# Kernel tuning notes

Measured on AMD Instinct MI355X. Metric: run time of the kernel, lower is better.

The kernel has to match this reference:

```python
import jax, jax.numpy as jnp
import numpy as np
from jax import lax

N = 4096   # total tree nodes in the forest
K = 8      # max children per side (left / right)
D = 512    # lstm_hid_dims (node embedding / enc output dim)
H = 512    # chain_hid_dims (chain LSTM hidden dim)


def _make_children(seed):
    # child indices strictly less than the parent index -> ascending node
    # order is a valid post-order (children encoded before parents).
    r = np.random.default_rng(seed)
    ch = np.full((N, K), -1, np.int64)
    for i in range(1, N):
        n = int(r.integers(0, K + 1))
        if n > 0:
            ch[i, :n] = r.integers(0, i, size=n)
    return jnp.asarray(ch)


def setup_inputs() -> dict:
    key = jax.random.key(0)
    ks = jax.random.split(key, 12)
    s = 1.0 / np.sqrt(H)
    f32 = jnp.float32
    return {
        "x0": jax.random.normal(ks[0], (N, D), f32),
        "Wl_ih": jax.random.normal(ks[1], (4 * H, D), f32) * s,
        "Wl_hh": jax.random.normal(ks[2], (4 * H, H), f32) * s,
        "bl_ih": jax.random.normal(ks[3], (4 * H,), f32) * s,
        "bl_hh": jax.random.normal(ks[4], (4 * H,), f32) * s,
        "Wr_ih": jax.random.normal(ks[5], (4 * H, D), f32) * s,
        "Wr_hh": jax.random.normal(ks[6], (4 * H, H), f32) * s,
        "br_ih": jax.random.normal(ks[7], (4 * H,), f32) * s,
        "br_hh": jax.random.normal(ks[8], (4 * H,), f32) * s,
        "W_enc": jax.random.normal(ks[9], (D, 2 * H), f32) * s,
        "b_enc": jax.random.normal(ks[10], (D,), f32) * s,
        "left_children": _make_children(1),
        "right_children": _make_children(2),
    }


def _lstm_chain(x_seq, mask, Wih, Whh, bih, bhh):
    """Masked torch-style LSTM over x_seq [L, D]; returns last valid hidden [H]."""
    def step(carry, xm):
        h, c = carry
        x, m = xm
        g = x @ Wih.T + bih + h @ Whh.T + bhh  # [4H], gate order i,f,g,o
        i, f, gg, o = jnp.split(g, 4)
        c_new = jax.nn.sigmoid(f) * c + jax.nn.sigmoid(i) * jnp.tanh(gg)
        h_new = jax.nn.sigmoid(o) * jnp.tanh(c_new)
        h = jnp.where(m, h_new, h)
        c = jnp.where(m, c_new, c)
        return (h, c), None

    z = jnp.zeros((H,), x_seq.dtype)
    (h, _), _ = lax.scan(step, (z, z), (x_seq, mask))
    return h


def reference(x0, Wl_ih, Wl_hh, bl_ih, bl_hh, Wr_ih, Wr_hh, br_ih, br_hh,
              W_enc, b_enc, left_children, right_children):
    # Bottom-up pass: process nodes in post-order (ascending index). For each
    # node: left-chain LSTM over [own embedding, left child encodings...],
    # right-chain likewise, then enc = tanh(Linear(concat(hl, hr))).
    def node_step(ctx, inputs):
        i, xi, lch, rch = inputs
        lmask = lch >= 0
        rmask = rch >= 0
        lvecs = jnp.where(lmask[:, None], ctx[jnp.clip(lch, 0)], 0.0)  # [K, D]
        rvecs = jnp.where(rmask[:, None], ctx[jnp.clip(rch, 0)], 0.0)
        true1 = jnp.ones((1,), bool)
        hl = _lstm_chain(jnp.concatenate([xi[None], lvecs], 0),
                         jnp.concatenate([true1, lmask]),
                         Wl_ih, Wl_hh, bl_ih, bl_hh)
        hr = _lstm_chain(jnp.concatenate([xi[None], rvecs], 0),
                         jnp.concatenate([true1, rmask]),
                         Wr_ih, Wr_hh, br_ih, br_hh)
        enc = jnp.tanh(jnp.concatenate([hl, hr]) @ W_enc.T + b_enc)  # [D]
        return ctx.at[i].set(enc), None

    ctx0 = jnp.zeros((N, D), x0.dtype)
    idx = jnp.arange(N)
    ctx, _ = lax.scan(node_step, ctx0, (idx, x0, left_children, right_children))
    return ctx  # [N, D] per-node encodings (context_vec after bottom_up)
```

## Files before the change

kernel.cpp:

```cpp
#include <hip/hip_runtime.h>
#include <math.h>

#define NN 4096
#define KK 8
#define DD 512
#define HH 512
#define NB 256
#define TPB 1024
#define NXCD 8
#define MAXT 4096
#define ENTCAP 40960
#define ENCCAP 16384
#define NNHH ((size_t)NN * HH)

typedef float v2f __attribute__((ext_vector_type(2)));

#define OFF_CTRL 0
#define OFF_HDR  8192
#define OFF_TCNT (OFF_HDR + 256)
#define OFF_TOFF (OFF_TCNT + 4 * MAXT)
#define OFF_TCUR (OFF_TOFF + 4 * MAXT)
#define OFF_ECNT (OFF_TCUR + 4 * MAXT)
#define OFF_EOFF (OFF_ECNT + 4 * MAXT)
#define OFF_ECUR (OFF_EOFF + 4 * MAXT)
#define OFF_LIST (OFF_ECUR + 4 * MAXT)
#define OFF_XL   (OFF_LIST + 4 * ENTCAP)
#define OFF_XR   (OFF_XL + 4 * ENTCAP)
#define OFF_ENC  (OFF_XR + 4 * ENTCAP)
#define OFF_H    (OFF_ENC + 4 * ENCCAP)
#define OFF_C    (OFF_H + 4 * 2 * 2 * NN * HH)
#define WS_ZERO_BYTES 8192

__device__ __forceinline__ float fast_tanh2x(float two_x) {
    return 1.0f - 2.0f * __builtin_amdgcn_rcpf(__expf(two_x) + 1.0f);
}

__device__ __forceinline__ void glds16(const float* g, float* l) {
    typedef __attribute__((address_space(1))) const void GV;
    typedef __attribute__((address_space(3))) void LV;
    __builtin_amdgcn_global_load_lds((GV*)g, (LV*)l, 16, 0, 0);
}

__device__ __forceinline__ void coh_store(float* p, float v) {
    __hip_atomic_store(p, v, __ATOMIC_RELAXED, __HIP_MEMORY_SCOPE_AGENT);
}
__device__ __forceinline__ v2f ldb2(const float* p) {
    unsigned long long raw = __hip_atomic_load((const unsigned long long*)p,
                                               __ATOMIC_RELAXED, __HIP_MEMORY_SCOPE_AGENT);
    union { unsigned long long u; v2f f; } c; c.u = raw; return c.f;
}

__global__ void __launch_bounds__(1024)
sched_kernel(const int* __restrict__ lch, const int* __restrict__ rch, char* ws) {
    const int t = threadIdx.x;
    int* hdr   = (int*)(ws + OFF_HDR);
    int* gcnt  = (int*)(ws + OFF_TCNT);
    int* goff  = (int*)(ws + OFF_TOFF);
    int* gcur  = (int*)(ws + OFF_TCUR);
    int* gecnt = (int*)(ws + OFF_ECNT);
    int* geoff = (int*)(ws + OFF_EOFF);
    int* gecur = (int*)(ws + OFF_ECUR);
    int* list  = (int*)(ws + OFF_LIST);
    int* xl    = (int*)(ws + OFF_XL);
    int* xr    = (int*)(ws + OFF_XR);
    int* enc   = (int*)(ws + OFF_ENC);

    __shared__ int s_meta[NN];
    __shared__ int s_start[NN];
    __shared__ int s_seg[1024];
    __shared__ int s_un, s_nt;

    for (int j = t; j < MAXT; j += 1024) { gcnt[j] = 0; gcur[j] = 0; gecnt[j] = 0; gecur[j] = 0; }
    if (t == 0) s_nt = 0;
    for (int i = t; i < NN; i += 1024) {
        int ll = 1, lr = 1; bool has = false;
#pragma unroll
        for (int k = 0; k < KK; ++k) {
            if (lch[i * KK + k] >= 0) { ll = k + 2; has = true; }
            if (rch[i * KK + k] >= 0) { lr = k + 2; has = true; }
        }
        const int L = ll > lr ? ll : lr;
        s_meta[i]  = ll | (lr << 4) | (L << 8);
        s_start[i] = has ? -1 : 0;
    }
    __syncthreads();

    for (;;) {
        if (t == 0) s_un = 0;
        __syncthreads();
        int myUn = 0;
        for (int i = t; i < NN; i += 1024) {
            if (s_start[i] < 0) {
                int mx = 0; bool ok = true;
#pragma unroll
                for (int k = 0; k < KK; ++k) {
                    int c = lch[i * KK + k];
                    if (c >= 0) {
                        const int st = s_start[c];
                        if (st < 0) ok = false;
                        else { const int v = st + ((s_meta[c] >> 8) & 0xF) - k; if (v > mx) mx = v; }
                    }
                    c = rch[i * KK + k];
                    if (c >= 0) {
                        const int st = s_start[c];
                        if (st < 0) ok = false;
                        else { const int v = st + ((s_meta[c] >> 8) & 0xF) - k; if (v > mx) mx = v; }
                    }
                }
                if (ok) s_start[i] = mx; else ++myUn;
            }
        }
        if (myUn) atomicAdd(&s_un, myUn);
        __syncthreads();
        if (s_un == 0) break;
        __syncthreads();
    }

    for (int i = t; i < NN; i += 1024)
        atomicMax(&s_nt, s_start[i] + ((s_meta[i] >> 8) & 0xF) + 1);
    __syncthreads();
    const int nt = s_nt;
    if (t == 0) hdr[0] = nt;
    for (int i = t; i < NN; i += 1024) {
        const int s = s_start[i], L = (s_meta[i] >> 8) & 0xF;
        for (int q = 0; q < L; ++q) atomicAdd(&gcnt[s + q], 1);
        atomicAdd(&gecnt[s + L], 1);
    }
    __syncthreads();

    auto scan4 = [&](int* cnt, int* off) {
        const int per = (nt + 1023) >> 10;
        const int lo = t * per, hi = (lo + per < nt) ? lo + per : nt;
        int sum = 0;
        for (int j = lo; j < hi; ++j) sum += (cnt[j] + 3) & ~3;
        s_seg[t] = sum;
        __syncthreads();
        if (t == 0) { int run = 0; for (int k = 0; k < 1024; ++k) { const int v = s_seg[k]; s_seg[k] = run; run += v; } }
        __syncthreads();
        int run = s_seg[t];
        for (int j = lo; j < hi; ++j) { off[j] = run; run += (cnt[j] + 3) & ~3; }
        __syncthreads();
    };
    scan4(gcnt, goff);
    scan4(gecnt, geoff);

    for (int i = t; i < NN; i += 1024) {
        const int m = s_meta[i], s = s_start[i];
        const int ll = m & 0xF, lr = (m >> 4) & 0xF, L = (m >> 8) & 0xF;
        for (int q = 0; q < L; ++q) {
            const int pos = goff[s + q] + atomicAdd(&gcur[s + q], 1);
            list[pos] = i | (q << 12) | (ll << 16) | (lr << 20);
            xl[pos] = (q == 0) ? i : ((q < ll) ? lch[i * KK + q - 1] : -1);
            xr[pos] = (q == 0) ? i : ((q < lr) ? rch[i * KK + q - 1] : -1);
        }
        const int ep = geoff[s + L] + atomicAdd(&gecur[s + L], 1);
        enc[ep] = i | (ll << 12) | (lr << 16);
    }
}

__device__ __forceinline__ void grid_barrier(int* ctrl, int blk, int xcd, int target) {
    __syncthreads();
    if (blk == 0) {
        const int t = threadIdx.x;
        if (t < 64) {
            if (t == 0)
                __hip_atomic_store(ctrl + 0, target, __ATOMIC_RELAXED, __HIP_MEMORY_SCOPE_AGENT);
            int spin = 0;
            for (;;) {
                const int m0 = __hip_atomic_load(ctrl + t * 4 + 0, __ATOMIC_RELAXED, __HIP_MEMORY_SCOPE_AGENT);
                const int m1 = __hip_atomic_load(ctrl + t * 4 + 1, __ATOMIC_RELAXED, __HIP_MEMORY_SCOPE_AGENT);
                const int m2 = __hip_atomic_load(ctrl + t * 4 + 2, __ATOMIC_RELAXED, __HIP_MEMORY_SCOPE_AGENT);
                const int m3 = __hip_atomic_load(ctrl + t * 4 + 3, __ATOMIC_RELAXED, __HIP_MEMORY_SCOPE_AGENT);
                const bool ok = (m0 >= target) & (m1 >= target) & (m2 >= target) & (m3 >= target);
                if (__all(ok)) break;
                if (++spin > 64) __builtin_amdgcn_s_sleep(16);
                else             __builtin_amdgcn_s_sleep(1);
            }
            if (t < NXCD)
                __hip_atomic_store(ctrl + 512 + t * 16, target, __ATOMIC_RELAXED, __HIP_MEMORY_SCOPE_AGENT);
        }
    } else {
        if (threadIdx.x == 0) {
            __hip_atomic_store(ctrl + blk, target, __ATOMIC_RELAXED, __HIP_MEMORY_SCOPE_AGENT);
            int spin = 0;
            while (__hip_atomic_load(ctrl + 512 + xcd * 16, __ATOMIC_RELAXED, __HIP_MEMORY_SCOPE_AGENT) < target) {
                if (++spin > 64) __builtin_amdgcn_s_sleep(16);
                else             __builtin_amdgcn_s_sleep(1);
            }
        }
    }
    __syncthreads();
}

__global__ void __launch_bounds__(TPB, 1)
tree_lstm_kernel(const float* __restrict__ x0,
                 const float* __restrict__ Wl_ih, const float* __restrict__ Wl_hh,
                 const float* __restrict__ bl_ih, const float* __restrict__ bl_hh,
                 const float* __restrict__ Wr_ih, const float* __restrict__ Wr_hh,
                 const float* __restrict__ br_ih, const float* __restrict__ br_hh,
                 const float* __restrict__ W_enc, const float* __restrict__ b_enc,
                 float* ctx, char* ws) {
    const int tid  = threadIdx.x;
    const int wv   = tid >> 6;
    const int wave = (blockIdx.x * TPB + tid) >> 6;
    const int lane = tid & 63;
    const int u    = wave & 511;
    const int side = (wave >> 9) & 1;
    const int p    = (wave >> 10) & 3;
    const int egrp = (wave >> 9) & 7;
    const int xcd  = blockIdx.x & (NXCD - 1);
    const int u0b  = (blockIdx.x * 16) & 511;

    int*   ctrl  = (int*)(ws + OFF_CTRL);
    int*   hdr   = (int*)(ws + OFF_HDR);
    int*   gcnt  = (int*)(ws + OFF_TCNT);
    int*   goff  = (int*)(ws + OFF_TOFF);
    int*   gecnt = (int*)(ws + OFF_ECNT);
    int*   geoff = (int*)(ws + OFF_EOFF);
    int*   list  = (int*)(ws + OFF_LIST);
    int*   xlidx = (int*)(ws + OFF_XL);
    int*   xridx = (int*)(ws + OFF_XR);
    int*   encl  = (int*)(ws + OFF_ENC);
    float* hbuf  = (float*)(ws + OFF_H);
    float* cbuf  = (float*)(ws + OFF_C);

    __shared__ float s_x[2][8][512];
    __shared__ float s_h[2][8][512];
    __shared__ float s_c[2][8][16];
    __shared__ float s_pad[5120];

    const float* Wih = side ? Wr_ih : Wl_ih;
    const float* Whh = side ? Wr_hh : Wl_hh;
    const float* bih = side ? br_ih : bl_ih;
    const float* bhh = side ? br_hh : bl_hh;

    v2f wih2[4][4], whh2[4][4];
#pragma unroll
    for (int g = 0; g < 4; ++g) {
        const size_t row = (size_t)g * HH + u;
        const float4 wa = *(const float4*)(Wih + row * DD + lane * 4);
        const float4 wb = *(const float4*)(Wih + row * DD + 256 + lane * 4);
        wih2[g][0] = (v2f){wa.x, wa.y}; wih2[g][1] = (v2f){wa.z, wa.w};
        wih2[g][2] = (v2f){wb.x, wb.y}; wih2[g][3] = (v2f){wb.z, wb.w};
        const float4 ha = *(const float4*)(Whh + row * HH + lane * 4);
        const float4 hb = *(const float4*)(Whh + row * HH + 256 + lane * 4);
        whh2[g][0] = (v2f){ha.x, ha.y}; whh2[g][1] = (v2f){ha.z, ha.w};
        whh2[g][2] = (v2f){hb.x, hb.y}; whh2[g][3] = (v2f){hb.z, hb.w};
    }
    const float bsumL = bih[(size_t)(lane & 3) * HH + u] + bhh[(size_t)(lane & 3) * HH + u];
    v2f wenc2[8];
#pragma unroll
    for (int j = 0; j < 4; ++j) {
        const float4 t = *(const float4*)(W_enc + (size_t)u * (2 * HH) + lane * 16 + j * 4);
        wenc2[j * 2 + 0] = (v2f){t.x, t.y};
        wenc2[j * 2 + 1] = (v2f){t.z, t.w};
    }
    const float bencv = b_enc[u];

    float* cb = cbuf + (size_t)side * NNHH;
    const int* xq = side ? xridx : xlidx;
    const int nt = hdr[0];
    if (nt < 0) ((volatile float*)s_pad)[tid] = 0.f;
    int bnum = 0;

    for (int tk = 0; tk < nt; ++tk) {
        const int cnt  = gcnt[tk],  off  = goff[tk];
        const int ecnt = gecnt[tk], eoff = geoff[tk];
        const int limit = off + cnt;

        const int slotBase = off + p * 8;
        const int nch = (limit > slotBase) ? ((limit - slotBase + 31) >> 5) : 0;

        v2f ph0, ph1, ph2, ph3, pc;
        bool pact = false;

        auto issue = [&](int buf, int chS) {
            pact = false;
            if (wv < 8) {
                const int e = chS + wv;
                if (e < limit) {
                    const int ent  = list[e];
                    const int q    = (ent >> 12) & 0xF;
                    const int xsrc = xq[e];
                    if (xsrc >= 0) {
                        const float* xrow = ((q == 0) ? x0 : ctx) + (size_t)xsrc * DD + lane * 4;
                        glds16(xrow,       &s_x[buf][wv][0]);
                        glds16(xrow + 256, &s_x[buf][wv][256]);
                        if (q > 0) {
                            pact = true;
                            const int i = ent & 0xFFF;
                            const float* hr = hbuf + (size_t)(((q & 1) ^ 1) * 2 + side) * NNHH
                                            + (size_t)i * HH + lane * 4;
                            ph0 = ldb2(hr);       ph1 = ldb2(hr + 2);
                            ph2 = ldb2(hr + 256); ph3 = ldb2(hr + 258);
                            if (lane < 8)
                                pc = ldb2(cb + (size_t)i * HH + u0b + lane * 2);
                        }
                    }
                }
            }
        };
        auto writeb = [&](int buf) {
            if (pact) {
                *(v2f*)&s_h[buf][wv][lane * 4]       = ph0;
                *(v2f*)&s_h[buf][wv][lane * 4 + 2]   = ph1;
                *(v2f*)&s_h[buf][wv][lane * 4 + 256] = ph2;
                *(v2f*)&s_h[buf][wv][lane * 4 + 258] = ph3;
                if (lane < 8)
                    *(v2f*)&s_c[buf][wv][lane * 2] = pc;
            }
        };

        if (nch > 0) { issue(0, slotBase); writeb(0); }
        for (int c = 0; c < nch; ++c) {
            __syncthreads();
            const int chS = slotBase + (c << 5);
            if (c + 1 < nch) issue((c + 1) & 1, chS + 32);
            const int bb = c & 1;

            const int4 eA = *(const int4*)(list + chS);
            const int4 eB = *(const int4*)(list + chS + 4);
            const int4 cA = *(const int4*)(xq + chS);
            const int4 cB = *(const int4*)(xq + chS + 4);
            const int ei[8] = {eA.x, eA.y, eA.z, eA.w, eB.x, eB.y, eB.z, eB.w};
            const int ci[8] = {cA.x, cA.y, cA.z, cA.w, cB.x, cB.y, cB.z, cB.w};
            bool act[8];
#pragma unroll
            for (int j = 0; j < 8; ++j)
                act[j] = (chS + j < limit) && (ci[j] >= 0);

#pragma unroll
            for (int j = 0; j < 8; ++j) {
                if (!act[j]) continue;
                const int ent = ei[j];
                const int i   = ent & 0xFFF;
                const int qj  = (ent >> 12) & 0xF;
                const float cpj = (qj > 0) ? s_c[bb][j][wv] : 0.f;
                const float4 xa = *(const float4*)&s_x[bb][j][lane * 4];
                const float4 xc = *(const float4*)&s_x[bb][j][lane * 4 + 256];
                v2f xv0 = (v2f){xa.x, xa.y}, xv1 = (v2f){xa.z, xa.w};
                v2f xv2 = (v2f){xc.x, xc.y}, xv3 = (v2f){xc.z, xc.w};
                v2f A0 = wih2[0][0] * xv0 + wih2[0][1] * xv1 + wih2[0][2] * xv2 + wih2[0][3] * xv3;
                v2f A1 = wih2[1][0] * xv0 + wih2[1][1] * xv1 + wih2[1][2] * xv2 + wih2[1][3] * xv3;
                v2f A2 = wih2[2][0] * xv0 + wih2[2][1] * xv1 + wih2[2][2] * xv2 + wih2[2][3] * xv3;
                v2f A3 = wih2[3][0] * xv0 + wih2[3][1] * xv1 + wih2[3][2] * xv2 + wih2[3][3] * xv3;
                if (qj > 0) {
                    const float4 ha = *(const float4*)&s_h[bb][j][lane * 4];
                    const float4 hc = *(const float4*)&s_h[bb][j][lane * 4 + 256];
                    v2f hv0 = (v2f){ha.x, ha.y}, hv1 = (v2f){ha.z, ha.w};
                    v2f hv2 = (v2f){hc.x, hc.y}, hv3 = (v2f){hc.z, hc.w};
                    A0 += whh2[0][0] * hv0 + whh2[0][1] * hv1 + whh2[0][2] * hv2 + whh2[0][3] * hv3;
                    A1 += whh2[1][0] * hv0 + whh2[1][1] * hv1 + whh2[1][2] * hv2 + whh2[1][3] * hv3;
                    A2 += whh2[2][0] * hv0 + whh2[2][1] * hv1 + whh2[2][2] * hv2 + whh2[2][3] * hv3;
                    A3 += whh2[3][0] * hv0 + whh2[3][1] * hv1 + whh2[3][2] * hv2 + whh2[3][3] * hv3;
                }
                float a0 = A0[0] + A0[1], a1 = A1[0] + A1[1];
                float a2 = A2[0] + A2[1], a3 = A3[0] + A3[1];
                float v01, v23, v;
                {
                    const bool hi = lane & 1;
                    float keep = hi ? a1 : a0, send = hi ? a0 : a1;
                    v01 = keep + __shfl_xor(send, 1, 64);
                    keep = hi ? a3 : a2; send = hi ? a2 : a3;
                    v23 = keep + __shfl_xor(send, 1, 64);
                }
                {
                    const bool hi = lane & 2;
                    const float keep = hi ? v23 : v01, send = hi ? v01 : v23;
                    v = keep + __shfl_xor(send, 2, 64);
                }
                v += __shfl_xor(v, 4, 64);
                v += __shfl_xor(v, 8, 64);
                v += __shfl_xor(v, 16, 64);
                v += __shfl_xor(v, 32, 64);
                const float gate = v + bsumL;
                const bool  isG  = (lane & 3) == 2;
                const float th   = fast_tanh2x(isG ? (gate + gate) : gate);
                const float tl   = isG ? th : 0.5f * (th + 1.0f);
                const float ti = __shfl(tl, 0, 64);
                const float tf = __shfl(tl, 1, 64);
                const float tg = __shfl(tl, 2, 64);
                const float to = __shfl(tl, 3, 64);
                const float cn = tf * cpj + ti * tg;
                const float hn = to * fast_tanh2x(cn + cn);
                if (lane == 0) {
                    coh_store(cb + (size_t)i * HH + u, cn);
                    coh_store(hbuf + (size_t)((qj & 1) * 2 + side) * NNHH + (size_t)i * HH + u, hn);
                }
            }
            if (c + 1 < nch) writeb((c + 1) & 1);
        }

        if (ecnt > 0) {
            const int lhalf = lane >> 5;
            const int col   = (lane * 16) & 511;
            const int elim  = eoff + ecnt;
            for (int slot = eoff + egrp; slot < elim; slot += 8) {
                const int e   = encl[slot];
                const int i   = e & 0xFFF;
                const int len = (e >> (12 + 4 * lhalf)) & 0xF;
                const float* hv = hbuf + (size_t)(((len - 1) & 1) * 2 + lhalf) * NNHH
                                + (size_t)i * HH + col;
                v2f acc2 = {0.f, 0.f};
#pragma unroll
                for (int k = 0; k < 8; ++k)
                    acc2 += wenc2[k] * ldb2(hv + k * 2);
                float acc = acc2[0] + acc2[1];
#pragma unroll
                for (int m = 1; m < 64; m <<= 1) acc += __shfl_xor(acc, m, 64);
                if (lane == 0)
                    coh_store(&ctx[(size_t)i * DD + u], fast_tanh2x(2.0f * (acc + bencv)));
            }
        }
        grid_barrier(ctrl, blockIdx.x, xcd, ++bnum);
    }
}

extern "C" void kernel_launch(void* const* d_in, const int* in_sizes, int n_in,
                              void* d_out, int out_size, void* d_ws, size_t ws_size,
                              hipStream_t stream) {
    hipMemsetAsync(d_ws, 0, WS_ZERO_BYTES, stream);
    sched_kernel<<<dim3(1), dim3(1024), 0, stream>>>(
        (const int*)d_in[11], (const int*)d_in[12], (char*)d_ws);
    tree_lstm_kernel<<<dim3(NB), dim3(TPB), 0, stream>>>(
        (const float*)d_in[0],
        (const float*)d_in[1], (const float*)d_in[2],
        (const float*)d_in[3], (const float*)d_in[4],
        (const float*)d_in[5], (const float*)d_in[6],
        (const float*)d_in[7], (const float*)d_in[8],
        (const float*)d_in[9], (const float*)d_in[10],
        (float*)d_out, (char*)d_ws);
}
```

Measured before the change: 13.66 ms.

## Replace global grid barrier with per-node progress flags for dataflow synchronization

Removes the per-tick grid-wide barrier and replaces it with fine-grained per-node progress counters. Each of 32 row blocks publishes chain-step and encoding completion per node, and consumers spin only on the flags for the specific node and child they need. This is meant to let fast blocks run ahead instead of waiting for every block each tick. In exchange it adds many spin loops with relaxed atomics, a larger zeroed workspace region, and a risk of memory-ordering issues because the flag stores are relaxed.

```diff
diff --git a/kernel.cpp b/kernel.cpp
--- a/kernel.cpp
+++ b/kernel.cpp
@@ -7,7 +7,6 @@
 #define HH 512
 #define NB 256
 #define TPB 1024
-#define NXCD 8
 #define MAXT 4096
 #define ENTCAP 40960
 #define ENCCAP 16384
@@ -15,8 +14,10 @@
 
 typedef float v2f __attribute__((ext_vector_type(2)));
 
-#define OFF_CTRL 0
-#define OFF_HDR  8192
+#define OFF_PROG  0
+#define OFF_CPROG (OFF_PROG + 4 * NN * 2 * 32)
+#define WS_ZERO_BYTES (OFF_CPROG + 4 * NN * 32)
+#define OFF_HDR  WS_ZERO_BYTES
 #define OFF_TCNT (OFF_HDR + 256)
 #define OFF_TOFF (OFF_TCNT + 4 * MAXT)
 #define OFF_TCUR (OFF_TOFF + 4 * MAXT)
@@ -29,7 +30,6 @@
 #define OFF_ENC  (OFF_XR + 4 * ENTCAP)
 #define OFF_H    (OFF_ENC + 4 * ENCCAP)
 #define OFF_C    (OFF_H + 4 * 2 * 2 * NN * HH)
-#define WS_ZERO_BYTES 8192
 
 __device__ __forceinline__ float fast_tanh2x(float two_x) {
     return 1.0f - 2.0f * __builtin_amdgcn_rcpf(__expf(two_x) + 1.0f);
@@ -48,6 +48,12 @@
     unsigned long long raw = __hip_atomic_load((const unsigned long long*)p,
                                                __ATOMIC_RELAXED, __HIP_MEMORY_SCOPE_AGENT);
     union { unsigned long long u; v2f f; } c; c.u = raw; return c.f;
+}
+__device__ __forceinline__ int ldf(const int* p) {
+    return __hip_atomic_load(p, __ATOMIC_RELAXED, __HIP_MEMORY_SCOPE_AGENT);
+}
+__device__ __forceinline__ void stf(int* p, int v) {
+    __hip_atomic_store(p, v, __ATOMIC_RELAXED, __HIP_MEMORY_SCOPE_AGENT);
 }
 
 __global__ void __launch_bounds__(1024)
@@ -156,40 +162,6 @@
         const int ep = geoff[s + L] + atomicAdd(&gecur[s + L], 1);
         enc[ep] = i | (ll << 12) | (lr << 16);
     }
-}
-
-__device__ __forceinline__ void grid_barrier(int* ctrl, int blk, int xcd, int target) {
-    __syncthreads();
-    if (blk == 0) {
-        const int t = threadIdx.x;
-        if (t < 64) {
-            if (t == 0)
-                __hip_atomic_store(ctrl + 0, target, __ATOMIC_RELAXED, __HIP_MEMORY_SCOPE_AGENT);
-            int spin = 0;
-            for (;;) {
-                const int m0 = __hip_atomic_load(ctrl + t * 4 + 0, __ATOMIC_RELAXED, __HIP_MEMORY_SCOPE_AGENT);
-                const int m1 = __hip_atomic_load(ctrl + t * 4 + 1, __ATOMIC_RELAXED, __HIP_MEMORY_SCOPE_AGENT);
-                const int m2 = __hip_atomic_load(ctrl + t * 4 + 2, __ATOMIC_RELAXED, __HIP_MEMORY_SCOPE_AGENT);
-                const int m3 = __hip_atomic_load(ctrl + t * 4 + 3, __ATOMIC_RELAXED, __HIP_MEMORY_SCOPE_AGENT);
-                const bool ok = (m0 >= target) & (m1 >= target) & (m2 >= target) & (m3 >= target);
-                if (__all(ok)) break;
-                if (++spin > 64) __builtin_amdgcn_s_sleep(16);
-                else             __builtin_amdgcn_s_sleep(1);
-            }
-            if (t < NXCD)
-                __hip_atomic_store(ctrl + 512 + t * 16, target, __ATOMIC_RELAXED, __HIP_MEMORY_SCOPE_AGENT);
-        }
-    } else {
-        if (threadIdx.x == 0) {
-            __hip_atomic_store(ctrl + blk, target, __ATOMIC_RELAXED, __HIP_MEMORY_SCOPE_AGENT);
-            int spin = 0;
-            while (__hip_atomic_load(ctrl + 512 + xcd * 16, __ATOMIC_RELAXED, __HIP_MEMORY_SCOPE_AGENT) < target) {
-                if (++spin > 64) __builtin_amdgcn_s_sleep(16);
-                else             __builtin_amdgcn_s_sleep(1);
-            }
-        }
-    }
-    __syncthreads();
 }
 
 __global__ void __launch_bounds__(TPB, 1)
@@ -208,10 +180,11 @@
     const int side = (wave >> 9) & 1;
     const int p    = (wave >> 10) & 3;
     const int egrp = (wave >> 9) & 7;
-    const int xcd  = blockIdx.x & (NXCD - 1);
+    const int rblk = blockIdx.x & 31;
     const int u0b  = (blockIdx.x * 16) & 511;
 
-    int*   ctrl  = (int*)(ws + OFF_CTRL);
+    int*   prog  = (int*)(ws + OFF_PROG);
+    int*   cprog = (int*)(ws + OFF_CPROG);
     int*   hdr   = (int*)(ws + OFF_HDR);
     int*   gcnt  = (int*)(ws + OFF_TCNT);
     int*   goff  = (int*)(ws + OFF_TOFF);
@@ -261,7 +234,6 @@
     const int* xq = side ? xridx : xlidx;
     const int nt = hdr[0];
     if (nt < 0) ((volatile float*)s_pad)[tid] = 0.f;
-    int bnum = 0;
 
     for (int tk = 0; tk < nt; ++tk) {
         const int cnt  = gcnt[tk],  off  = goff[tk];
@@ -283,12 +255,36 @@
                     const int q    = (ent >> 12) & 0xF;
                     const int xsrc = xq[e];
                     if (xsrc >= 0) {
-                        const float* xrow = ((q == 0) ? x0 : ctx) + (size_t)xsrc * DD + lane * 4;
-                        glds16(xrow,       &s_x[buf][wv][0]);
-                        glds16(xrow + 256, &s_x[buf][wv][256]);
-                        if (q > 0) {
+                        if (q == 0) {
+                            const float* xrow = x0 + (size_t)xsrc * DD + lane * 4;
+                            glds16(xrow,       &s_x[buf][wv][0]);
+                            glds16(xrow + 256, &s_x[buf][wv][256]);
+                        } else {
+                            const int i = ent & 0xFFF;
+                            {
+                                const int* pf = prog + (size_t)(i * 2 + side) * 32;
+                                int spin = 0;
+                                for (;;) {
+                                    const int v = (lane < 32) ? ldf(pf + lane) : q;
+                                    if (__all(v >= q)) break;
+                                    if (++spin > 64) __builtin_amdgcn_s_sleep(16);
+                                    else             __builtin_amdgcn_s_sleep(1);
+                                }
+                            }
+                            {
+                                const int* cf = cprog + (size_t)xsrc * 32;
+                                int spin = 0;
+                                for (;;) {
+                                    const int v = (lane < 32) ? ldf(cf + lane) : 1;
+                                    if (__all(v >= 1)) break;
+                                    if (++spin > 64) __builtin_amdgcn_s_sleep(16);
+                                    else             __builtin_amdgcn_s_sleep(1);
+                                }
+                            }
                             pact = true;
-                            const int i = ent & 0xFFF;
+                            const float* xrow = ctx + (size_t)xsrc * DD + lane * 4;
+                            glds16(xrow,       &s_x[buf][wv][0]);
+                            glds16(xrow + 256, &s_x[buf][wv][256]);
                             const float* hr = hbuf + (size_t)(((q & 1) ^ 1) * 2 + side) * NNHH
                                             + (size_t)i * HH + lane * 4;
                             ph0 = ldb2(hr);       ph1 = ldb2(hr + 2);
@@ -310,10 +306,22 @@
                     *(v2f*)&s_c[buf][wv][lane * 2] = pc;
             }
         };
-
+        auto publish = [&](int chS) {
+            if (tid < 8) {
+                const int e = chS + tid;
+                if (e < limit) {
+                    const int ent = list[e];
+                    stf(prog + (size_t)((ent & 0xFFF) * 2 + side) * 32 + rblk,
+                        ((ent >> 12) & 0xF) + 1);
+                }
+            }
+        };
+
+        int chPrev = -1;
         if (nch > 0) { issue(0, slotBase); writeb(0); }
         for (int c = 0; c < nch; ++c) {
             __syncthreads();
+            if (chPrev >= 0) publish(chPrev);
             const int chS = slotBase + (c << 5);
             if (c + 1 < nch) issue((c + 1) & 1, chS + 32);
             const int bb = c & 1;
@@ -389,6 +397,11 @@
                 }
             }
             if (c + 1 < nch) writeb((c + 1) & 1);
+            chPrev = chS;
+        }
+        if (nch > 0) {
+            __syncthreads();
+            publish(chPrev);
         }
 
         if (ecnt > 0) {
@@ -398,6 +411,18 @@
             for (int slot = eoff + egrp; slot < elim; slot += 8) {
                 const int e   = encl[slot];
                 const int i   = e & 0xFFF;
+                const int ll  = (e >> 12) & 0xF, lr = (e >> 16) & 0xF;
+                {
+                    const int* pf = prog + (size_t)i * 64;
+                    const int need = (lane < 32) ? ll : lr;
+                    int spin = 0;
+                    for (;;) {
+                        const int v = ldf(pf + lane);
+                        if (__all(v >= need)) break;
+                        if (++spin > 64) __builtin_amdgcn_s_sleep(16);
+                        else             __builtin_amdgcn_s_sleep(1);
+                    }
+                }
                 const int len = (e >> (12 + 4 * lhalf)) & 0xF;
                 const float* hv = hbuf + (size_t)(((len - 1) & 1) * 2 + lhalf) * NNHH
                                 + (size_t)i * HH + col;
@@ -411,8 +436,10 @@
                 if (lane == 0)
                     coh_store(&ctx[(size_t)i * DD + u], fast_tanh2x(2.0f * (acc + bencv)));
             }
-        }
-        grid_barrier(ctrl, blockIdx.x, xcd, ++bnum);
+            __syncthreads();
+            for (int slot = eoff + egrp + 8 * tid; slot < elim; slot += 8 * TPB)
+                stf(cprog + (size_t)(encl[slot] & 0xFFF) * 32 + rblk, 1);
+        }
     }
 }
 
```

New measurement: 14.32 ms. +4.8%, slower.
